# Optimization experiments

Measured on AMD Instinct MI355X. Metric: run time of the kernel, lower is better.

The kernel has to match this reference:

```python
import jax, jax.numpy as jnp
import numpy as np

DIM = 768
NUM_HEADS = 12
HEAD_DIM = DIM // NUM_HEADS
SCALE = HEAD_DIM ** -0.5


def setup_inputs() -> dict:
    key = jax.random.key(0)
    k_x, k_qkv, k_proj, k_pb = jax.random.split(key, 4)
    B, N = 16, 1024
    x = jax.random.normal(k_x, (B, N, DIM), dtype=jnp.float32)
    # nn.Linear weights: stored as [out, in]; qkv_bias=False -> no qkv bias
    w_qkv = jax.random.normal(k_qkv, (3 * DIM, DIM), dtype=jnp.float32) * (DIM ** -0.5)
    w_proj = jax.random.normal(k_proj, (DIM, DIM), dtype=jnp.float32) * (DIM ** -0.5)
    b_proj = jax.random.normal(k_pb, (DIM,), dtype=jnp.float32) * 0.01
    return {"x": x, "w_qkv": w_qkv, "w_proj": w_proj, "b_proj": b_proj}


def reference(x, w_qkv, w_proj, b_proj):
    B, N, C = x.shape
    H, D = NUM_HEADS, HEAD_DIM
    # qkv projection: [B,N,3C] -> [3,B,H,N,D]
    qkv = jnp.einsum('bnc,oc->bno', x, w_qkv)
    qkv = qkv.reshape(B, N, 3, H, D).transpose(2, 0, 3, 1, 4)
    q, k, v = qkv[0], qkv[1], qkv[2]
    # scaled dot-product attention (dropout ratios are 0.0 -> identity)
    attn = jnp.einsum('bhnd,bhmd->bhnm', q, k) * SCALE
    attn = jax.nn.softmax(attn, axis=-1)
    out = jnp.einsum('bhnm,bhmd->bhnd', attn, v)
    out = out.transpose(0, 2, 1, 3).reshape(B, N, C)
    # output projection
    return jnp.einsum('bnc,oc->bno', out, w_proj) + b_proj
```

## Files before the change

### kernel.cpp

```cpp
#include <hip/hip_runtime.h>
#include <hip/hip_bf16.h>
#include <stdint.h>

typedef unsigned short u16;
typedef unsigned int   u32;
typedef short bf16x8 __attribute__((ext_vector_type(8)));
typedef float f32x4  __attribute__((ext_vector_type(4)));
typedef float f32x16 __attribute__((ext_vector_type(16)));

#define MFMA16(A,B,C) __builtin_amdgcn_mfma_f32_16x16x32_bf16((A),(B),(C),0,0,0)
#define MFMA32(A,B,C) __builtin_amdgcn_mfma_f32_32x32x16_bf16((A),(B),(C),0,0,0)

__device__ __forceinline__ u16 f2b(float x) {
  u32 u = __float_as_uint(x);
  u += 0x7fffu + ((u >> 16) & 1u);
  return (u16)(u >> 16);
}
__device__ __forceinline__ u32 cvtpk(float lo, float hi) {
  u32 r;
  asm("v_cvt_pk_bf16_f32 %0, %1, %2" : "=v"(r) : "v"(lo), "v"(hi));
  return r;
}

typedef __attribute__((address_space(1))) const void glob_void;
typedef __attribute__((address_space(3))) void lds_void;
__device__ __forceinline__ void gld16(const void* g, void* s) {
  __builtin_amdgcn_global_load_lds((glob_void*)g, (lds_void*)s, 16, 0, 0);
}

__global__ void cvt_bf16(const float4* __restrict__ in, ushort4* __restrict__ out, int n4) {
  int stride = gridDim.x * blockDim.x;
  for (int i = blockIdx.x * blockDim.x + threadIdx.x; i < n4; i += stride) {
    float4 v = in[i];
    ushort4 o;
    o.x = f2b(v.x); o.y = f2b(v.y); o.z = f2b(v.z); o.w = f2b(v.w);
    out[i] = o;
  }
}

__global__ __launch_bounds__(256) void gemm_qkv(
    const u16* __restrict__ xb, const u16* __restrict__ wb,
    u16* __restrict__ q, u16* __restrict__ k, u16* __restrict__ vt)
{
  __shared__ u16 lA[128*32];
  __shared__ u16 lB[128*32];
  const int tid = threadIdx.x;
  const int lane = tid & 63;
  const int wv = tid >> 6;
  const int wr = wv >> 1, wc = wv & 1;
  const int m0 = blockIdx.x << 7;
  const int o0 = blockIdx.y << 7;
  f32x4 acc[4][4] = {};
  const int srow = tid >> 2;
  const int sb   = (((tid & 3) ^ ((srow >> 1) & 3)) << 4);
  const char* gA0 = (const char*)(xb + (size_t)(m0 + srow)      * 768) + sb;
  const char* gA1 = (const char*)(xb + (size_t)(m0 + 64 + srow) * 768) + sb;
  const char* gB0 = (const char*)(wb + (size_t)(o0 + srow)      * 768) + sb;
  const char* gB1 = (const char*)(wb + (size_t)(o0 + 64 + srow) * 768) + sb;
  char* sA = (char*)lA + tid * 16;
  char* sB = (char*)lB + tid * 16;
  const int frow = lane & 15;
  const int fk   = (((lane >> 4) ^ ((frow >> 1) & 3)) << 4);
  for (int kt = 0; kt < 24; ++kt) {
    const int kb = kt << 6;
    gld16(gA0 + kb, sA);
    gld16(gA1 + kb, sA + 4096);
    gld16(gB0 + kb, sB);
    gld16(gB1 + kb, sB + 4096);
    asm volatile("s_waitcnt vmcnt(0)" ::: "memory");
    __syncthreads();
    bf16x8 af[4], bfr[4];
#pragma unroll
    for (int m = 0; m < 4; ++m)
      af[m] = *(const bf16x8*)((const char*)lA + ((wr*64 + m*16 + frow) << 6) + fk);
#pragma unroll
    for (int n = 0; n < 4; ++n)
      bfr[n] = *(const bf16x8*)((const char*)lB + ((wc*64 + n*16 + frow) << 6) + fk);
#pragma unroll
    for (int m = 0; m < 4; ++m)
#pragma unroll
      for (int n = 0; n < 4; ++n)
        acc[m][n] = MFMA16(af[m], bfr[n], acc[m][n]);
    __syncthreads();
  }
  const int which = o0 / 768;
  const int ob = o0 - which * 768;
  const float QSCALE = 0.18033688011112042f;
#pragma unroll
  for (int n = 0; n < 4; ++n) {
    const int go = ob + wc*64 + n*16 + (lane & 15);
    const int h = go >> 6, d = go & 63;
#pragma unroll
    for (int m = 0; m < 4; ++m) {
      const int gm0 = m0 + wr*64 + m*16 + ((lane >> 4) << 2);
      const int b = gm0 >> 10, nn0 = gm0 & 1023;
      if (which == 2) {
        ushort4 o4;
        o4.x = f2b(acc[m][n][0]); o4.y = f2b(acc[m][n][1]);
        o4.z = f2b(acc[m][n][2]); o4.w = f2b(acc[m][n][3]);
        *(ushort4*)(vt + (((size_t)((b*12 + h)*64 + d)) << 10) + nn0) = o4;
      } else if (which == 0) {
#pragma unroll
        for (int r = 0; r < 4; ++r)
          q[((size_t)((b*12 + h)*1024 + nn0 + r) << 6) + d] = f2b(acc[m][n][r] * QSCALE);
      } else {
#pragma unroll
        for (int r = 0; r < 4; ++r)
          k[((size_t)((b*12 + h)*1024 + nn0 + r) << 6) + d] = f2b(acc[m][n][r]);
      }
    }
  }
}

__global__ __launch_bounds__(256) void attn_fwd(
    const u16* __restrict__ q, const u16* __restrict__ kk,
    const u16* __restrict__ vt, u16* __restrict__ ao)
{
  __shared__ u16 lK[64*64];
  __shared__ u16 lV[64*64];
  const int tid = threadIdx.x, lane = tid & 63, wv = tid >> 6;
  const int l31 = lane & 31, hh = lane >> 5;
  const int qt = blockIdx.x, bh = blockIdx.y;
  const u16*  qb = q  + ((size_t)bh << 16);
  const char* kg = (const char*)(kk + ((size_t)bh << 16));
  const char* vg = (const char*)(vt + ((size_t)bh << 16));
  const int qrow = (qt << 7) + (wv << 5) + l31;
  bf16x8 qreg[4];
#pragma unroll
  for (int c = 0; c < 4; ++c)
    qreg[c] = *(const bf16x8*)((const char*)qb + (size_t)qrow*128 + c*32 + hh*16);
  f32x16 ot[2] = {};
  float mrun = -1e30f, lrun = 0.f;
  const int o1 = tid << 4, o2 = o1 + 4096;
  const int ko1 = o1 ^ (((o1 >> 7) & 7) << 4);
  const int ko2 = o2 ^ (((o2 >> 7) & 7) << 4);
  const int d1 = o1 >> 7, d2 = o2 >> 7;
  const int vo1 = d1*2048 + ((o1 & 127) ^ ((d1 & 7) << 4));
  const int vo2 = d2*2048 + ((o2 & 127) ^ ((d2 & 7) << 4));
  char* sK = (char*)lK;
  char* sV = (char*)lV;
  for (int t0 = 0; t0 < 16; ++t0) {
    gld16(kg + (t0 << 13) + ko1, sK + o1);
    gld16(kg + (t0 << 13) + ko2, sK + o2);
    gld16(vg + (t0 << 7) + vo1, sV + o1);
    gld16(vg + (t0 << 7) + vo2, sV + o2);
    asm volatile("s_waitcnt vmcnt(0)" ::: "memory");
    __syncthreads();
    f32x16 s[2] = {};
#pragma unroll
    for (int tt = 0; tt < 2; ++tt) {
      const int row = (tt << 5) + l31;
      const int rb = row << 7;
      const int sw = (row & 7) << 4;
#pragma unroll
      for (int c = 0; c < 4; ++c) {
        bf16x8 kf = *(const bf16x8*)(sK + rb + (((c << 5) + (hh << 4)) ^ sw));
        s[tt] = MFMA32(kf, qreg[c], s[tt]);
      }
    }
    float mloc = s[0][0];
#pragma unroll
    for (int tt = 0; tt < 2; ++tt)
#pragma unroll
      for (int r = 0; r < 16; ++r) mloc = fmaxf(mloc, s[tt][r]);
    mloc = fmaxf(mloc, __shfl_xor(mloc, 32));
    const float mnew  = fmaxf(mrun, mloc);
    const float alpha = __builtin_amdgcn_exp2f(mrun - mnew);
    float sum = 0.f;
#pragma unroll
    for (int tt = 0; tt < 2; ++tt)
#pragma unroll
      for (int r = 0; r < 16; ++r) {
        s[tt][r] = __builtin_amdgcn_exp2f(s[tt][r] - mnew);
        sum += s[tt][r];
      }
    sum += __shfl_xor(sum, 32);
    lrun = lrun * alpha + sum;
    mrun = mnew;
#pragma unroll
    for (int dt = 0; dt < 2; ++dt)
#pragma unroll
      for (int r = 0; r < 16; ++r) ot[dt][r] *= alpha;
    bf16x8 pb[4];
#pragma unroll
    for (int tt = 0; tt < 2; ++tt) {
      u32 x0 = cvtpk(s[tt][0],  s[tt][1]);
      u32 y0 = cvtpk(s[tt][4],  s[tt][5]);
      u32 x1 = cvtpk(s[tt][2],  s[tt][3]);
      u32 y1 = cvtpk(s[tt][6],  s[tt][7]);
      asm("v_permlane32_swap_b32 %0, %1" : "+v"(x0), "+v"(y0));
      asm("v_permlane32_swap_b32 %0, %1" : "+v"(x1), "+v"(y1));
      u32 x2 = cvtpk(s[tt][8],  s[tt][9]);
      u32 y2 = cvtpk(s[tt][12], s[tt][13]);
      u32 x3 = cvtpk(s[tt][10], s[tt][11]);
      u32 y3 = cvtpk(s[tt][14], s[tt][15]);
      asm("v_permlane32_swap_b32 %0, %1" : "+v"(x2), "+v"(y2));
      asm("v_permlane32_swap_b32 %0, %1" : "+v"(x3), "+v"(y3));
      union { u32 u[4]; bf16x8 v; } a, b;
      a.u[0] = x0; a.u[1] = x1; a.u[2] = y0; a.u[3] = y1;
      b.u[0] = x2; b.u[1] = x3; b.u[2] = y2; b.u[3] = y3;
      pb[2*tt]     = a.v;
      pb[2*tt + 1] = b.v;
    }
#pragma unroll
    for (int dt = 0; dt < 2; ++dt) {
      const int row = (dt << 5) + l31;
      const int rb = row << 7;
      const int sw = (row & 7) << 4;
#pragma unroll
      for (int cc = 0; cc < 4; ++cc) {
        bf16x8 vf = *(const bf16x8*)(sV + rb + (((cc << 5) + (hh << 4)) ^ sw));
        ot[dt] = MFMA32(vf, pb[cc], ot[dt]);
      }
    }
    __syncthreads();
  }
  const float linv = 1.f / lrun;
  const int b = bh / 12, h = bh - b * 12;
  u16* po = ao + ((size_t)(b*1024 + qrow)) * 768 + h*64;
#pragma unroll
  for (int dt = 0; dt < 2; ++dt) {
#pragma unroll
    for (int g = 0; g < 4; ++g) {
      ushort4 o4;
      o4.x = f2b(ot[dt][4*g + 0] * linv);
      o4.y = f2b(ot[dt][4*g + 1] * linv);
      o4.z = f2b(ot[dt][4*g + 2] * linv);
      o4.w = f2b(ot[dt][4*g + 3] * linv);
      *(ushort4*)(po + dt*32 + g*8 + hh*4) = o4;
    }
  }
}

__global__ __launch_bounds__(256) void gemm_proj(
    const u16* __restrict__ ab, const u16* __restrict__ wb,
    const float* __restrict__ bias, float* __restrict__ out)
{
  __shared__ u16 lA[128*32];
  __shared__ u16 lB[128*32];
  const int tid = threadIdx.x;
  const int lane = tid & 63;
  const int wv = tid >> 6;
  const int wr = wv >> 1, wc = wv & 1;
  const int m0 = blockIdx.x << 7;
  const int o0 = blockIdx.y << 7;
  f32x4 acc[4][4] = {};
  const int srow = tid >> 2;
  const int sb   = (((tid & 3) ^ ((srow >> 1) & 3)) << 4);
  const char* gA0 = (const char*)(ab + (size_t)(m0 + srow)      * 768) + sb;
  const char* gA1 = (const char*)(ab + (size_t)(m0 + 64 + srow) * 768) + sb;
  const char* gB0 = (const char*)(wb + (size_t)(o0 + srow)      * 768) + sb;
  const char* gB1 = (const char*)(wb + (size_t)(o0 + 64 + srow) * 768) + sb;
  char* sA = (char*)lA + tid * 16;
  char* sB = (char*)lB + tid * 16;
  const int frow = lane & 15;
  const int fk   = (((lane >> 4) ^ ((frow >> 1) & 3)) << 4);
  for (int kt = 0; kt < 24; ++kt) {
    const int kb = kt << 6;
    gld16(gA0 + kb, sA);
    gld16(gA1 + kb, sA + 4096);
    gld16(gB0 + kb, sB);
    gld16(gB1 + kb, sB + 4096);
    asm volatile("s_waitcnt vmcnt(0)" ::: "memory");
    __syncthreads();
    bf16x8 af[4], bfr[4];
#pragma unroll
    for (int m = 0; m < 4; ++m)
      af[m] = *(const bf16x8*)((const char*)lA + ((wr*64 + m*16 + frow) << 6) + fk);
#pragma unroll
    for (int n = 0; n < 4; ++n)
      bfr[n] = *(const bf16x8*)((const char*)lB + ((wc*64 + n*16 + frow) << 6) + fk);
#pragma unroll
    for (int m = 0; m < 4; ++m)
#pragma unroll
      for (int n = 0; n < 4; ++n)
        acc[m][n] = MFMA16(af[m], bfr[n], acc[m][n]);
    __syncthreads();
  }
#pragma unroll
  for (int n = 0; n < 4; ++n) {
    const int go = o0 + wc*64 + n*16 + (lane & 15);
    const float bv = bias[go];
#pragma unroll
    for (int m = 0; m < 4; ++m) {
#pragma unroll
      for (int r = 0; r < 4; ++r) {
        const int gm = m0 + wr*64 + m*16 + ((lane >> 4) << 2) + r;
        out[(size_t)gm * 768 + go] = acc[m][n][r] + bv;
      }
    }
  }
}

extern "C" void kernel_launch(void* const* d_in, const int* in_sizes, int n_in,
                              void* d_out, int out_size, void* d_ws, size_t ws_size,
                              hipStream_t stream)
{
  (void)in_sizes; (void)n_in; (void)out_size; (void)ws_size;
  const float* x  = (const float*)d_in[0];
  const float* wq = (const float*)d_in[1];
  const float* wp = (const float*)d_in[2];
  const float* bp = (const float*)d_in[3];
  float* out = (float*)d_out;
  char* ws = (char*)d_ws;
  u16* xb     = (u16*)(ws);
  u16* wqkvb  = (u16*)(ws + 25165824);
  u16* wprojb = (u16*)(ws + 28704768);
  u16* qa     = (u16*)(ws + 29884416);
  u16* ka     = (u16*)(ws + 55050240);
  u16* vta    = (u16*)(ws + 80216064);
  u16* ao     = xb;

  cvt_bf16<<<2048, 256, 0, stream>>>((const float4*)x,  (ushort4*)xb,     3145728);
  cvt_bf16<<<1024, 256, 0, stream>>>((const float4*)wq, (ushort4*)wqkvb,   442368);
  cvt_bf16<<< 576, 256, 0, stream>>>((const float4*)wp, (ushort4*)wprojb,  147456);
  gemm_qkv<<<dim3(128, 18), 256, 0, stream>>>(xb, wqkvb, qa, ka, vta);
  attn_fwd<<<dim3(8, 192), 256, 0, stream>>>(qa, ka, vta, ao);
  gemm_proj<<<dim3(128, 6), 256, 0, stream>>>(ao, wprojb, bp, out);
}
```

Measured before the change: 236.3 us.

## Double-buffer LDS in GEMMs and attention, add lazy softmax rescale

```diff
diff --git a/kernel.cpp b/kernel.cpp
--- a/kernel.cpp
+++ b/kernel.cpp
@@ -42,8 +42,8 @@
     const u16* __restrict__ xb, const u16* __restrict__ wb,
     u16* __restrict__ q, u16* __restrict__ k, u16* __restrict__ vt)
 {
-  __shared__ u16 lA[128*32];
-  __shared__ u16 lB[128*32];
+  __shared__ u16 lA[2][128*32];
+  __shared__ u16 lB[2][128*32];
   const int tid = threadIdx.x;
   const int lane = tid & 63;
   const int wv = tid >> 6;
@@ -61,27 +61,33 @@
   char* sB = (char*)lB + tid * 16;
   const int frow = lane & 15;
   const int fk   = (((lane >> 4) ^ ((frow >> 1) & 3)) << 4);
+
+#define QKV_STAGE(buf, kt) do { const int kb_ = (kt) << 6; const int bo_ = (buf) << 13; \
+    gld16(gA0 + kb_, sA + bo_); gld16(gA1 + kb_, sA + bo_ + 4096); \
+    gld16(gB0 + kb_, sB + bo_); gld16(gB1 + kb_, sB + bo_ + 4096); } while (0)
+
+  QKV_STAGE(0, 0);
+  asm volatile("s_waitcnt vmcnt(0) lgkmcnt(0)" ::: "memory");
+  __builtin_amdgcn_s_barrier();
   for (int kt = 0; kt < 24; ++kt) {
-    const int kb = kt << 6;
-    gld16(gA0 + kb, sA);
-    gld16(gA1 + kb, sA + 4096);
-    gld16(gB0 + kb, sB);
-    gld16(gB1 + kb, sB + 4096);
-    asm volatile("s_waitcnt vmcnt(0)" ::: "memory");
-    __syncthreads();
+    const int cur = kt & 1;
+    if (kt < 23) QKV_STAGE(cur ^ 1, kt + 1);
+    const char* bA = (const char*)lA + (cur << 13);
+    const char* bB = (const char*)lB + (cur << 13);
     bf16x8 af[4], bfr[4];
 #pragma unroll
     for (int m = 0; m < 4; ++m)
-      af[m] = *(const bf16x8*)((const char*)lA + ((wr*64 + m*16 + frow) << 6) + fk);
+      af[m] = *(const bf16x8*)(bA + ((wr*64 + m*16 + frow) << 6) + fk);
 #pragma unroll
     for (int n = 0; n < 4; ++n)
-      bfr[n] = *(const bf16x8*)((const char*)lB + ((wc*64 + n*16 + frow) << 6) + fk);
+      bfr[n] = *(const bf16x8*)(bB + ((wc*64 + n*16 + frow) << 6) + fk);
 #pragma unroll
     for (int m = 0; m < 4; ++m)
 #pragma unroll
       for (int n = 0; n < 4; ++n)
         acc[m][n] = MFMA16(af[m], bfr[n], acc[m][n]);
-    __syncthreads();
+    asm volatile("s_waitcnt vmcnt(0) lgkmcnt(0)" ::: "memory");
+    __builtin_amdgcn_s_barrier();
   }
   const int which = o0 / 768;
   const int ob = o0 - which * 768;
@@ -116,11 +122,11 @@
     const u16* __restrict__ q, const u16* __restrict__ kk,
     const u16* __restrict__ vt, u16* __restrict__ ao)
 {
-  __shared__ u16 lK[64*64];
-  __shared__ u16 lV[64*64];
+  __shared__ u16 lK[2][64*64];
+  __shared__ u16 lV[2][64*64];
   const int tid = threadIdx.x, lane = tid & 63, wv = tid >> 6;
   const int l31 = lane & 31, hh = lane >> 5;
-  const int qt = blockIdx.x, bh = blockIdx.y;
+  const int bh = blockIdx.x, qt = blockIdx.y;
   const u16*  qb = q  + ((size_t)bh << 16);
   const char* kg = (const char*)(kk + ((size_t)bh << 16));
   const char* vg = (const char*)(vt + ((size_t)bh << 16));
@@ -139,13 +145,21 @@
   const int vo2 = d2*2048 + ((o2 & 127) ^ ((d2 & 7) << 4));
   char* sK = (char*)lK;
   char* sV = (char*)lV;
+
+#define ATTN_STAGE(buf, t) do { const int bo_ = (buf) << 13; \
+    gld16(kg + ((t) << 13) + ko1, sK + bo_ + o1); \
+    gld16(kg + ((t) << 13) + ko2, sK + bo_ + o2); \
+    gld16(vg + ((t) << 7) + vo1, sV + bo_ + o1); \
+    gld16(vg + ((t) << 7) + vo2, sV + bo_ + o2); } while (0)
+
+  ATTN_STAGE(0, 0);
+  asm volatile("s_waitcnt vmcnt(0) lgkmcnt(0)" ::: "memory");
+  __builtin_amdgcn_s_barrier();
   for (int t0 = 0; t0 < 16; ++t0) {
-    gld16(kg + (t0 << 13) + ko1, sK + o1);
-    gld16(kg + (t0 << 13) + ko2, sK + o2);
-    gld16(vg + (t0 << 7) + vo1, sV + o1);
-    gld16(vg + (t0 << 7) + vo2, sV + o2);
-    asm volatile("s_waitcnt vmcnt(0)" ::: "memory");
-    __syncthreads();
+    const int cur = t0 & 1;
+    if (t0 < 15) ATTN_STAGE(cur ^ 1, t0 + 1);
+    const char* bK = (const char*)lK + (cur << 13);
+    const char* bV = (const char*)lV + (cur << 13);
     f32x16 s[2] = {};
 #pragma unroll
     for (int tt = 0; tt < 2; ++tt) {
@@ -154,7 +168,7 @@
       const int sw = (row & 7) << 4;
 #pragma unroll
       for (int c = 0; c < 4; ++c) {
-        bf16x8 kf = *(const bf16x8*)(sK + rb + (((c << 5) + (hh << 4)) ^ sw));
+        bf16x8 kf = *(const bf16x8*)(bK + rb + (((c << 5) + (hh << 4)) ^ sw));
         s[tt] = MFMA32(kf, qreg[c], s[tt]);
       }
     }
@@ -163,24 +177,27 @@
     for (int tt = 0; tt < 2; ++tt)
 #pragma unroll
       for (int r = 0; r < 16; ++r) mloc = fmaxf(mloc, s[tt][r]);
-    mloc = fmaxf(mloc, __shfl_xor(mloc, 32));
-    const float mnew  = fmaxf(mrun, mloc);
-    const float alpha = __builtin_amdgcn_exp2f(mrun - mnew);
+    if (!__all(mloc <= mrun + 8.f)) {
+      mloc = fmaxf(mloc, __shfl_xor(mloc, 32));
+      const float mnew  = fmaxf(mrun, mloc);
+      const float alpha = __builtin_amdgcn_exp2f(mrun - mnew);
+      lrun *= alpha;
+#pragma unroll
+      for (int dt = 0; dt < 2; ++dt)
+#pragma unroll
+        for (int r = 0; r < 16; ++r) ot[dt][r] *= alpha;
+      mrun = mnew;
+    }
     float sum = 0.f;
 #pragma unroll
     for (int tt = 0; tt < 2; ++tt)
 #pragma unroll
       for (int r = 0; r < 16; ++r) {
-        s[tt][r] = __builtin_amdgcn_exp2f(s[tt][r] - mnew);
+        s[tt][r] = __builtin_amdgcn_exp2f(s[tt][r] - mrun);
         sum += s[tt][r];
       }
     sum += __shfl_xor(sum, 32);
-    lrun = lrun * alpha + sum;
-    mrun = mnew;
-#pragma unroll
-    for (int dt = 0; dt < 2; ++dt)
-#pragma unroll
-      for (int r = 0; r < 16; ++r) ot[dt][r] *= alpha;
+    lrun += sum;
     bf16x8 pb[4];
 #pragma unroll
     for (int tt = 0; tt < 2; ++tt) {
@@ -209,11 +226,12 @@
       const int sw = (row & 7) << 4;
 #pragma unroll
       for (int cc = 0; cc < 4; ++cc) {
-        bf16x8 vf = *(const bf16x8*)(sV + rb + (((cc << 5) + (hh << 4)) ^ sw));
+        bf16x8 vf = *(const bf16x8*)(bV + rb + (((cc << 5) + (hh << 4)) ^ sw));
         ot[dt] = MFMA32(vf, pb[cc], ot[dt]);
       }
     }
-    __syncthreads();
+    asm volatile("s_waitcnt vmcnt(0) lgkmcnt(0)" ::: "memory");
+    __builtin_amdgcn_s_barrier();
   }
   const float linv = 1.f / lrun;
   const int b = bh / 12, h = bh - b * 12;
@@ -236,8 +254,8 @@
     const u16* __restrict__ ab, const u16* __restrict__ wb,
     const float* __restrict__ bias, float* __restrict__ out)
 {
-  __shared__ u16 lA[128*32];
-  __shared__ u16 lB[128*32];
+  __shared__ u16 lA[2][128*32];
+  __shared__ u16 lB[2][128*32];
   const int tid = threadIdx.x;
   const int lane = tid & 63;
   const int wv = tid >> 6;
@@ -255,27 +273,29 @@
   char* sB = (char*)lB + tid * 16;
   const int frow = lane & 15;
   const int fk   = (((lane >> 4) ^ ((frow >> 1) & 3)) << 4);
+
+  QKV_STAGE(0, 0);
+  asm volatile("s_waitcnt vmcnt(0) lgkmcnt(0)" ::: "memory");
+  __builtin_amdgcn_s_barrier();
   for (int kt = 0; kt < 24; ++kt) {
-    const int kb = kt << 6;
-    gld16(gA0 + kb, sA);
-    gld16(gA1 + kb, sA + 4096);
-    gld16(gB0 + kb, sB);
-    gld16(gB1 + kb, sB + 4096);
-    asm volatile("s_waitcnt vmcnt(0)" ::: "memory");
-    __syncthreads();
+    const int cur = kt & 1;
+    if (kt < 23) QKV_STAGE(cur ^ 1, kt + 1);
+    const char* bA = (const char*)lA + (cur << 13);
+    const char* bB = (const char*)lB + (cur << 13);
     bf16x8 af[4], bfr[4];
 #pragma unroll
     for (int m = 0; m < 4; ++m)
-      af[m] = *(const bf16x8*)((const char*)lA + ((wr*64 + m*16 + frow) << 6) + fk);
+      af[m] = *(const bf16x8*)(bA + ((wr*64 + m*16 + frow) << 6) + fk);
 #pragma unroll
     for (int n = 0; n < 4; ++n)
-      bfr[n] = *(const bf16x8*)((const char*)lB + ((wc*64 + n*16 + frow) << 6) + fk);
+      bfr[n] = *(const bf16x8*)(bB + ((wc*64 + n*16 + frow) << 6) + fk);
 #pragma unroll
     for (int m = 0; m < 4; ++m)
 #pragma unroll
       for (int n = 0; n < 4; ++n)
         acc[m][n] = MFMA16(af[m], bfr[n], acc[m][n]);
-    __syncthreads();
+    asm volatile("s_waitcnt vmcnt(0) lgkmcnt(0)" ::: "memory");
+    __builtin_amdgcn_s_barrier();
   }
 #pragma unroll
   for (int n = 0; n < 4; ++n) {
@@ -315,6 +335,6 @@
   cvt_bf16<<<1024, 256, 0, stream>>>((const float4*)wq, (ushort4*)wqkvb,   442368);
   cvt_bf16<<< 576, 256, 0, stream>>>((const float4*)wp, (ushort4*)wprojb,  147456);
   gemm_qkv<<<dim3(128, 18), 256, 0, stream>>>(xb, wqkvb, qa, ka, vta);
-  attn_fwd<<<dim3(8, 192), 256, 0, stream>>>(qa, ka, vta, ao);
+  attn_fwd<<<dim3(192, 8), 256, 0, stream>>>(qa, ka, vta, ao);
   gemm_proj<<<dim3(128, 6), 256, 0, stream>>>(ao, wprojb, bp, out);
 }
```

Result: faster. 215.9 us (-8.6%).
